# Optimization experiments

Hardware: AMD Instinct MI355X
Metric: run time of the kernel (lower is better)

The kernel has to match this reference:

```python
import jax, jax.numpy as jnp
import numpy as np

D_MODEL = 2048
NUM_HEADS = 16
NUM_KV_HEADS = 4
D_HEAD = D_MODEL // NUM_HEADS  # 128
GROUPS = NUM_HEADS // NUM_KV_HEADS  # 4
ROPE_THETA = 10000.0
EPS = 1e-6


def setup_inputs() -> dict:
    key = jax.random.key(0)
    ks = jax.random.split(key, 7)
    B, S = 2, 2048
    s = 1.0 / np.sqrt(D_MODEL)
    return {
        "qkv": jax.random.normal(ks[0], (B, S, D_MODEL), dtype=jnp.float32),
        "Wq": jax.random.normal(ks[1], (D_MODEL, D_MODEL), dtype=jnp.float32) * s,
        "Wk": jax.random.normal(ks[2], (NUM_KV_HEADS * D_HEAD, D_MODEL), dtype=jnp.float32) * s,
        "Wv": jax.random.normal(ks[3], (NUM_KV_HEADS * D_HEAD, D_MODEL), dtype=jnp.float32) * s,
        "Wo": jax.random.normal(ks[4], (D_MODEL, D_MODEL), dtype=jnp.float32) * s,
        "q_gamma": jnp.ones((D_HEAD,), dtype=jnp.float32),
        "k_gamma": jnp.ones((D_HEAD,), dtype=jnp.float32),
    }


def _rmsnorm(x, gamma):
    # per-head RMSNorm over last dim (d_head)
    var = jnp.mean(jnp.square(x), axis=-1, keepdims=True)
    return x * jax.lax.rsqrt(var + EPS) * gamma


def _rope(x, cos, sin):
    # x: [B, S, H, Dh]; cos/sin: [S, Dh]
    half = x.shape[-1] // 2
    x1, x2 = x[..., :half], x[..., half:]
    rot = jnp.concatenate([-x2, x1], axis=-1)
    return x * cos[None, :, None, :] + rot * sin[None, :, None, :]


def reference(qkv, Wq, Wk, Wv, Wo, q_gamma, k_gamma):
    B, S, D = qkv.shape
    q = jnp.einsum("bsd,ed->bse", qkv, Wq).reshape(B, S, NUM_HEADS, D_HEAD)
    k = jnp.einsum("bsd,ed->bse", qkv, Wk).reshape(B, S, NUM_KV_HEADS, D_HEAD)
    v = jnp.einsum("bsd,ed->bse", qkv, Wv).reshape(B, S, NUM_KV_HEADS, D_HEAD)

    q = _rmsnorm(q, q_gamma)
    k = _rmsnorm(k, k_gamma)

    # RoPE, position_ids = arange(S)
    pos = jnp.arange(S, dtype=jnp.float32)
    inv_freq = 1.0 / (ROPE_THETA ** (jnp.arange(0, D_HEAD, 2, dtype=jnp.float32) / D_HEAD))
    ang = pos[:, None] * inv_freq[None, :]                 # [S, Dh/2]
    cos = jnp.concatenate([jnp.cos(ang), jnp.cos(ang)], axis=-1)  # [S, Dh]
    sin = jnp.concatenate([jnp.sin(ang), jnp.sin(ang)], axis=-1)
    q = _rope(q, cos, sin)
    k = _rope(k, cos, sin)

    # [B, H, S, Dh]
    q = q.transpose(0, 2, 1, 3)
    k = k.transpose(0, 2, 1, 3)
    v = v.transpose(0, 2, 1, 3)
    # GQA: repeat kv heads
    k = jnp.repeat(k, GROUPS, axis=1)
    v = jnp.repeat(v, GROUPS, axis=1)

    scale = 1.0 / np.sqrt(D_HEAD)
    scores = jnp.einsum("bhqd,bhkd->bhqk", q, k) * scale
    causal = jnp.tril(jnp.ones((S, S), dtype=bool))
    scores = jnp.where(causal[None, None], scores, jnp.finfo(scores.dtype).min)
    probs = jax.nn.softmax(scores, axis=-1)
    attended = jnp.einsum("bhqk,bhkd->bhqd", probs, v)     # [B, H, S, Dh]
    attended = attended.transpose(0, 2, 1, 3).reshape(B, S, D)
    return jnp.einsum("bsd,ed->bse", attended, Wo)
```

## Files before the change

kernel.cpp:

```cpp
#include <hip/hip_runtime.h>

#define S_LEN 2048
#define B_SZ 2
#define DMODEL 2048
#define NHEADS 16
#define NKV 4
#define DHEAD 128
#define SCALE 0.08838834764831845f
#define KVB 32

typedef __bf16 bf16x8 __attribute__((ext_vector_type(8)));
typedef __bf16 bf16x4 __attribute__((ext_vector_type(4)));
typedef float f32x4 __attribute__((ext_vector_type(4)));

#define MFMA(a, b, c) __builtin_amdgcn_mfma_f32_16x16x32_bf16(a, b, c, 0, 0, 0)

__device__ __forceinline__ void gload_lds16(const __bf16* g, __bf16* l) {
    __builtin_amdgcn_global_load_lds(
        (const __attribute__((address_space(1))) unsigned int*)g,
        (__attribute__((address_space(3))) unsigned int*)l, 16, 0, 0);
}

__global__ void rope_tables_kernel(float* __restrict__ cosT, float* __restrict__ sinT) {
    int i = blockIdx.x * 256 + threadIdx.x;
    int s = i >> 6, d = i & 63;
    float freq = powf(10000.0f, -(2.0f * (float)d) / 128.0f);
    float ang = (float)s * freq;
    cosT[i] = cosf(ang);
    sinT[i] = sinf(ang);
}

__global__ __launch_bounds__(256) void convert_kernel(
    const float* __restrict__ s0, const float* __restrict__ s1,
    const float* __restrict__ s2, const float* __restrict__ s3,
    const float* __restrict__ s4,
    __bf16* __restrict__ d0, __bf16* __restrict__ d1, __bf16* __restrict__ d2,
    __bf16* __restrict__ d3, __bf16* __restrict__ d4) {
    const float* s;
    __bf16* d;
    int n8;
    switch (blockIdx.y) {
        case 0: s = s0; d = d0; n8 = (B_SZ * S_LEN * DMODEL) / 8; break;
        case 1: s = s1; d = d1; n8 = (DMODEL * DMODEL) / 8; break;
        case 2: s = s2; d = d2; n8 = (NKV * DHEAD * DMODEL) / 8; break;
        case 3: s = s3; d = d3; n8 = (NKV * DHEAD * DMODEL) / 8; break;
        default: s = s4; d = d4; n8 = (DMODEL * DMODEL) / 8; break;
    }
    for (int i = blockIdx.x * 256 + threadIdx.x; i < n8; i += 512 * 256) {
        float4 a = ((const float4*)s)[2 * i];
        float4 b = ((const float4*)s)[2 * i + 1];
        bf16x8 o = {(__bf16)a.x, (__bf16)a.y, (__bf16)a.z, (__bf16)a.w,
                    (__bf16)b.x, (__bf16)b.y, (__bf16)b.z, (__bf16)b.w};
        *(bf16x8*)&d[i * 8] = o;
    }
}

__device__ __forceinline__ void gemm_bt_bf16(const __bf16* __restrict__ A,
                                             const __bf16* __restrict__ W,
                                             float* __restrict__ C, int ldc,
                                             int bm, int bn, int K) {
    __shared__ alignas(16) __bf16 As[2][128][32];
    __shared__ alignas(16) __bf16 Bs[2][128][32];
    const int tid = threadIdx.x;
    const int lane = tid & 63;
    const int wave = tid >> 6;
    const int lr = lane & 15;
    const int lk = lane >> 4;
    const int wm = (wave >> 1) * 64;
    const int wn = (wave & 1) * 64;
    const int srow = lane >> 2;
    const int sc8 = (lane & 3) * 8;

    auto stage = [&](int bi, int k0) {
#pragma unroll
        for (int i = 0; i < 2; ++i) {
            const int row = i * 64 + wave * 16 + srow;
            gload_lds16(A + (size_t)(bm + row) * K + k0 + sc8,
                        &As[bi][0][0] + i * 2048 + wave * 512);
            gload_lds16(W + (size_t)(bn + row) * K + k0 + sc8,
                        &Bs[bi][0][0] + i * 2048 + wave * 512);
        }
    };

    f32x4 acc[4][4] = {};
    const int NT = K >> 5;

    stage(0, 0);
    __syncthreads();
    for (int t = 0; t < NT; ++t) {
        if (t + 1 < NT) stage((t + 1) & 1, (t + 1) * 32);
        const int bi = t & 1;
        bf16x8 af[4], bfr[4];
#pragma unroll
        for (int i = 0; i < 4; ++i) {
            af[i]  = *(const bf16x8*)&As[bi][wm + i * 16 + lr][lk * 8];
            bfr[i] = *(const bf16x8*)&Bs[bi][wn + i * 16 + lr][lk * 8];
        }
#pragma unroll
        for (int mi = 0; mi < 4; ++mi)
#pragma unroll
            for (int ni = 0; ni < 4; ++ni)
                acc[mi][ni] = MFMA(af[mi], bfr[ni], acc[mi][ni]);
        __syncthreads();
    }

#pragma unroll
    for (int mi = 0; mi < 4; ++mi)
#pragma unroll
        for (int ni = 0; ni < 4; ++ni)
#pragma unroll
            for (int r = 0; r < 4; ++r) {
                int row = bm + wm + mi * 16 + lk * 4 + r;
                int col = bn + wn + ni * 16 + lr;
                C[(size_t)row * ldc + col] = acc[mi][ni][r];
            }
}

__global__ __launch_bounds__(256) void qkv_proj_kernel(
    const __bf16* __restrict__ qkvb, const __bf16* __restrict__ Wq,
    const __bf16* __restrict__ Wk, const __bf16* __restrict__ Wv,
    float* __restrict__ q_tmp, float* __restrict__ k_tmp, float* __restrict__ v_tmp) {
    int bm = blockIdx.x * 128;
    int ny = blockIdx.y;
    const __bf16* W;
    float* C;
    int ldc, bn;
    if (ny < 16)      { W = Wq; C = q_tmp; ldc = 2048; bn = ny * 128; }
    else if (ny < 20) { W = Wk; C = k_tmp; ldc = 512;  bn = (ny - 16) * 128; }
    else              { W = Wv; C = v_tmp; ldc = 512;  bn = (ny - 20) * 128; }
    gemm_bt_bf16(qkvb, W, C, ldc, bm, bn, 2048);
}

__global__ __launch_bounds__(256) void out_proj_kernel(
    const __bf16* __restrict__ att, const __bf16* __restrict__ Wo,
    float* __restrict__ out) {
    gemm_bt_bf16(att, Wo, out, 2048, blockIdx.x * 128, blockIdx.y * 128, 2048);
}

__global__ __launch_bounds__(256) void postproc_kernel(
    const float* __restrict__ q_tmp, const float* __restrict__ k_tmp,
    const float* __restrict__ qg, const float* __restrict__ kg,
    const float* __restrict__ cosT, const float* __restrict__ sinT,
    __bf16* __restrict__ qb, __bf16* __restrict__ kb) {
    int bs = blockIdx.x;
    int b = bs >> 11, s = bs & 2047;
    int wave = threadIdx.x >> 6, lane = threadIdx.x & 63;
    float c  = cosT[s * 64 + lane];
    float sn = sinT[s * 64 + lane];
    float g1q = qg[lane], g2q = qg[lane + 64];
    float g1k = kg[lane], g2k = kg[lane + 64];

    for (int h = wave; h < NHEADS; h += 4) {
        const float* row = q_tmp + (size_t)bs * 2048 + h * 128;
        float x1 = row[lane], x2 = row[lane + 64];
        float ss = x1 * x1 + x2 * x2;
#pragma unroll
        for (int m = 1; m < 64; m <<= 1) ss += __shfl_xor(ss, m);
        float rs = rsqrtf(ss * (1.0f / 128.0f) + 1e-6f);
        float n1 = x1 * rs * g1q, n2 = x2 * rs * g2q;
        float y1 = (n1 * c - n2 * sn) * SCALE;
        float y2 = (n2 * c + n1 * sn) * SCALE;
        __bf16* orow = qb + (((size_t)(b * NHEADS + h)) * S_LEN + s) * DHEAD;
        orow[lane] = (__bf16)y1;
        orow[lane + 64] = (__bf16)y2;
    }
    int h = wave;
    if (h < NKV) {
        const float* row = k_tmp + (size_t)bs * 512 + h * 128;
        float x1 = row[lane], x2 = row[lane + 64];
        float ss = x1 * x1 + x2 * x2;
#pragma unroll
        for (int m = 1; m < 64; m <<= 1) ss += __shfl_xor(ss, m);
        float rs = rsqrtf(ss * (1.0f / 128.0f) + 1e-6f);
        float n1 = x1 * rs * g1k, n2 = x2 * rs * g2k;
        float y1 = n1 * c - n2 * sn;
        float y2 = n2 * c + n1 * sn;
        __bf16* orow = kb + (((size_t)(b * NKV + h)) * S_LEN + s) * DHEAD;
        orow[lane] = (__bf16)y1;
        orow[lane + 64] = (__bf16)y2;
    }
}

__global__ __launch_bounds__(256) void v_transpose_kernel(
    const float* __restrict__ v_tmp, __bf16* __restrict__ vt) {
    int bkv = blockIdx.x;
    int b = bkv >> 2, kvh = bkv & 3;
    int s0 = blockIdx.y * 64, d0 = blockIdx.z * 64;
    __shared__ float tile[64][65];
#pragma unroll
    for (int i = 0; i < 16; ++i) {
        int idx = threadIdx.x + i * 256;
        int r = idx >> 6, cc = idx & 63;
        tile[r][cc] = v_tmp[((size_t)(b * S_LEN) + s0 + r) * 512 + kvh * 128 + d0 + cc];
    }
    __syncthreads();
#pragma unroll
    for (int i = 0; i < 16; ++i) {
        int idx = threadIdx.x + i * 256;
        int r = idx >> 6, cc = idx & 63;
        vt[((size_t)bkv * DHEAD + d0 + r) * S_LEN + s0 + cc] = (__bf16)tile[cc][r];
    }
}

__global__ __launch_bounds__(256, 2) void flash_kernel(
    const __bf16* __restrict__ qb, const __bf16* __restrict__ kb,
    const __bf16* __restrict__ vt, __bf16* __restrict__ att) {
    __shared__ alignas(16) __bf16 K_lds[2][32 * 128];
    __shared__ alignas(16) __bf16 V_lds[2][128 * 32];
    __shared__ alignas(16) __bf16 p_lds[4][16][40];

    const int bh = blockIdx.x;
    const int b = bh >> 4, h = bh & 15, kv = h >> 2;
    const int j = blockIdx.y;
    const int lane = threadIdx.x & 63, wave = threadIdx.x >> 6;
    const int lr = lane & 15, lk = lane >> 4;

    const int qloB = j * 64 + wave * 16;
    const int qhiB = (31 - j) * 64 + wave * 16;
    const int ntL  = ((qloB + 15) >> 5) + 1;
    const int ntHw = ((qhiB + 15) >> 5) + 1;
    const int ntH  = 64 - 2 * j;

    const __bf16* Qp = qb + ((size_t)(b * NHEADS + h)) * S_LEN * DHEAD;
    const __bf16* Kp = kb + ((size_t)(b * NKV + kv)) * S_LEN * DHEAD;
    const __bf16* Vt = vt + ((size_t)(b * NKV + kv)) * DHEAD * S_LEN;

    bf16x8 qlo[4], qhi[4];
#pragma unroll
    for (int f = 0; f < 4; ++f) {
        qlo[f] = *(const bf16x8*)&Qp[(size_t)(qloB + lr) * DHEAD + f * 32 + lk * 8];
        qhi[f] = *(const bf16x8*)&Qp[(size_t)(qhiB + lr) * DHEAD + f * 32 + lk * 8];
    }

    const int c0 = 2 * wave;
    const int l4 = lane >> 4, l15 = lane & 15;
    const int l2 = lane >> 2, l3 = lane & 3;
    const int vcol = ((l3 ^ (l2 & 3)) << 3);

    auto stage = [&](int bufi, int t) {
        const int k0s = t * KVB;
#pragma unroll
        for (int i = 0; i < 2; ++i) {
            const int c = c0 + i;
            const int rK = c * 4 + l4;
            const int kcol = ((l15 ^ (rK & 7)) << 3);
            gload_lds16(Kp + (size_t)(k0s + rK) * DHEAD + kcol, &K_lds[bufi][c * 512]);
            const int rV = c * 16 + l2;
            gload_lds16(Vt + (size_t)rV * S_LEN + k0s + vcol, &V_lds[bufi][c * 512]);
        }
    };

    f32x4 accL[8] = {}, accH[8] = {};
    float lsumL[4] = {0.f, 0.f, 0.f, 0.f}, lsumH[4] = {0.f, 0.f, 0.f, 0.f};
    const int swzK = (lr & 7) << 4;
    const int swzV = (lr & 3) << 4;

    auto frag_step = [&](const bf16x8 (&qf)[4], int qbase, f32x4 (&acc)[8],
                         float (&lsum)[4], const bf16x8 (&kf)[8],
                         const bf16x8 (&vf)[8], int k0) {
        f32x4 sc[2] = {};
#pragma unroll
        for (int kk = 0; kk < 2; ++kk)
#pragma unroll
            for (int f = 0; f < 4; ++f)
                sc[kk] = MFMA(qf[f], kf[kk * 4 + f], sc[kk]);
        asm volatile("s_waitcnt lgkmcnt(0)" ::: "memory");
#pragma unroll
        for (int r = 0; r < 4; ++r) {
            const int qr = qbase + lk * 4 + r;
            float s0 = sc[0][r], s1 = sc[1][r];
            if (k0 + lr > qr) s0 = -1e30f;
            if (k0 + 16 + lr > qr) s1 = -1e30f;
            float p0 = __expf(s0), p1 = __expf(s1);
            lsum[r] += p0 + p1;
            p_lds[wave][lk * 4 + r][lr] = (__bf16)p0;
            p_lds[wave][lk * 4 + r][lr + 16] = (__bf16)p1;
        }
        asm volatile("s_waitcnt lgkmcnt(0)" ::: "memory");
        bf16x8 pf = *(const bf16x8*)&p_lds[wave][lr][lk * 8];
#pragma unroll
        for (int nf = 0; nf < 8; ++nf)
            acc[nf] = MFMA(pf, vf[nf], acc[nf]);
    };

    int cur = 0;
    stage(0, 0);
    __syncthreads();
    for (int t = 0; t < ntH; ++t) {
        if (t + 1 < ntH) stage(cur ^ 1, t + 1);
        const int k0 = t * KVB;
        bf16x8 kf[8], vf[8];
#pragma unroll
        for (int kk = 0; kk < 2; ++kk)
#pragma unroll
            for (int f = 0; f < 4; ++f) {
                const int cb = (f * 64 + lk * 16) ^ swzK;
                kf[kk * 4 + f] =
                    *(const bf16x8*)((const char*)&K_lds[cur][(kk * 16 + lr) * 128] + cb);
            }
#pragma unroll
        for (int nf = 0; nf < 8; ++nf) {
            const int cb = (lk * 16) ^ swzV;
            vf[nf] = *(const bf16x8*)((const char*)&V_lds[cur][(nf * 16 + lr) * 32] + cb);
        }
        if (t < ntHw) frag_step(qhi, qhiB, accH, lsumH, kf, vf, k0);
        if (t < ntL)  frag_step(qlo, qloB, accL, lsumL, kf, vf, k0);
        __syncthreads();
        cur ^= 1;
    }

#pragma unroll
    for (int r = 0; r < 4; ++r) {
#pragma unroll
        for (int m = 1; m < 16; m <<= 1) {
            lsumL[r] += __shfl_xor(lsumL[r], m);
            lsumH[r] += __shfl_xor(lsumH[r], m);
        }
    }
#pragma unroll
    for (int nf = 0; nf < 8; ++nf)
#pragma unroll
        for (int r = 0; r < 4; ++r) {
            int qrL = qloB + lk * 4 + r;
            int qrH = qhiB + lk * 4 + r;
            att[((size_t)(b * S_LEN) + qrL) * DMODEL + h * DHEAD + nf * 16 + lr] =
                (__bf16)(accL[nf][r] / lsumL[r]);
            att[((size_t)(b * S_LEN) + qrH) * DMODEL + h * DHEAD + nf * 16 + lr] =
                (__bf16)(accH[nf][r] / lsumH[r]);
        }
}

extern "C" void kernel_launch(void* const* d_in, const int* in_sizes, int n_in,
                              void* d_out, int out_size, void* d_ws, size_t ws_size,
                              hipStream_t stream) {
    const float* qkv = (const float*)d_in[0];
    const float* Wq  = (const float*)d_in[1];
    const float* Wk  = (const float*)d_in[2];
    const float* Wv  = (const float*)d_in[3];
    const float* Wo  = (const float*)d_in[4];
    const float* qg  = (const float*)d_in[5];
    const float* kg  = (const float*)d_in[6];
    float* out = (float*)d_out;

    size_t off = 0;
    char* wsb = (char*)d_ws;
    auto alloc = [&](size_t n) {
        char* p = wsb + off;
        off += (n + 255) & ~(size_t)255;
        return (void*)p;
    };
    const size_t M = (size_t)B_SZ * S_LEN;
    float* cosT  = (float*)alloc((size_t)S_LEN * 64 * 4);
    float* sinT  = (float*)alloc((size_t)S_LEN * 64 * 4);
    float* q_tmp = (float*)alloc(M * 2048 * 4);
    float* k_tmp = (float*)alloc(M * 512 * 4);
    float* v_tmp = (float*)alloc(M * 512 * 4);
    __bf16* qb   = (__bf16*)alloc((size_t)B_SZ * NHEADS * S_LEN * DHEAD * 2);
    __bf16* kb   = (__bf16*)alloc((size_t)B_SZ * NKV * S_LEN * DHEAD * 2);
    __bf16* vt   = (__bf16*)alloc((size_t)B_SZ * NKV * DHEAD * S_LEN * 2);
    __bf16* att  = (__bf16*)alloc(M * DMODEL * 2);
    __bf16* wo_b = (__bf16*)alloc((size_t)DMODEL * DMODEL * 2);
    __bf16* qkv_b = att;
    __bf16* wq_b  = qb;
    __bf16* wk_b  = vt;
    __bf16* wv_b  = wk_b + (size_t)NKV * DHEAD * DMODEL;

    rope_tables_kernel<<<(S_LEN * 64) / 256, 256, 0, stream>>>(cosT, sinT);
    convert_kernel<<<dim3(512, 5), 256, 0, stream>>>(qkv, Wq, Wk, Wv, Wo,
                                                     qkv_b, wq_b, wk_b, wv_b, wo_b);
    qkv_proj_kernel<<<dim3(M / 128, 24), 256, 0, stream>>>(qkv_b, wq_b, wk_b, wv_b,
                                                           q_tmp, k_tmp, v_tmp);
    postproc_kernel<<<dim3(M), 256, 0, stream>>>(q_tmp, k_tmp, qg, kg, cosT, sinT, qb, kb);
    v_transpose_kernel<<<dim3(B_SZ * NKV, S_LEN / 64, DHEAD / 64), 256, 0, stream>>>(v_tmp, vt);
    flash_kernel<<<dim3(B_SZ * NHEADS, 16), 256, 0, stream>>>(qb, kb, vt, att);
    out_proj_kernel<<<dim3(M / 128, DMODEL / 128), 256, 0, stream>>>(att, wo_b, out);
}
```

Before: 230.9 us.

## Fuse RMSNorm, RoPE and V transpose into QKV projection epilogue

Changes the GEMM wave tiling from 2x2 (64x64 per wave) to 4x1, so each wave owns 32 full rows across all 128 columns, one complete head. That lets the QKV projection epilogue compute per-head RMSNorm and RoPE in registers and write bf16 Q/K, and write V directly transposed. This drops the fp32 q/k/v scratch round trip and the separate postproc and transpose kernels. Costs: each wave now loads all 8 B fragments per k-step (more LDS reads), the epilogue stores are scattered 2-byte writes, and workspace buffers are no longer aliased.

```diff
diff --git a/kernel.cpp b/kernel.cpp
--- a/kernel.cpp
+++ b/kernel.cpp
@@ -55,10 +55,10 @@
     }
 }
 
-__device__ __forceinline__ void gemm_bt_bf16(const __bf16* __restrict__ A,
-                                             const __bf16* __restrict__ W,
-                                             float* __restrict__ C, int ldc,
-                                             int bm, int bn, int K) {
+__device__ __forceinline__ void gemm_main(const __bf16* __restrict__ A,
+                                          const __bf16* __restrict__ W,
+                                          int bm, int bn, int K,
+                                          f32x4 (&acc)[2][8]) {
     __shared__ alignas(16) __bf16 As[2][128][32];
     __shared__ alignas(16) __bf16 Bs[2][128][32];
     const int tid = threadIdx.x;
@@ -66,8 +66,6 @@
     const int wave = tid >> 6;
     const int lr = lane & 15;
     const int lk = lane >> 4;
-    const int wm = (wave >> 1) * 64;
-    const int wn = (wave & 1) * 64;
     const int srow = lane >> 2;
     const int sc8 = (lane & 3) * 8;
 
@@ -82,124 +80,127 @@
         }
     };
 
-    f32x4 acc[4][4] = {};
+#pragma unroll
+    for (int mi = 0; mi < 2; ++mi)
+#pragma unroll
+        for (int ni = 0; ni < 8; ++ni) acc[mi][ni] = (f32x4){0.f, 0.f, 0.f, 0.f};
+
     const int NT = K >> 5;
-
     stage(0, 0);
     __syncthreads();
     for (int t = 0; t < NT; ++t) {
         if (t + 1 < NT) stage((t + 1) & 1, (t + 1) * 32);
         const int bi = t & 1;
-        bf16x8 af[4], bfr[4];
-#pragma unroll
-        for (int i = 0; i < 4; ++i) {
-            af[i]  = *(const bf16x8*)&As[bi][wm + i * 16 + lr][lk * 8];
-            bfr[i] = *(const bf16x8*)&Bs[bi][wn + i * 16 + lr][lk * 8];
-        }
-#pragma unroll
-        for (int mi = 0; mi < 4; ++mi)
-#pragma unroll
-            for (int ni = 0; ni < 4; ++ni)
+        bf16x8 af[2], bfr[8];
+#pragma unroll
+        for (int i = 0; i < 2; ++i)
+            af[i] = *(const bf16x8*)&As[bi][wave * 32 + i * 16 + lr][lk * 8];
+#pragma unroll
+        for (int i = 0; i < 8; ++i)
+            bfr[i] = *(const bf16x8*)&Bs[bi][i * 16 + lr][lk * 8];
+#pragma unroll
+        for (int mi = 0; mi < 2; ++mi)
+#pragma unroll
+            for (int ni = 0; ni < 8; ++ni)
                 acc[mi][ni] = MFMA(af[mi], bfr[ni], acc[mi][ni]);
         __syncthreads();
     }
-
-#pragma unroll
-    for (int mi = 0; mi < 4; ++mi)
-#pragma unroll
-        for (int ni = 0; ni < 4; ++ni)
-#pragma unroll
-            for (int r = 0; r < 4; ++r) {
-                int row = bm + wm + mi * 16 + lk * 4 + r;
-                int col = bn + wn + ni * 16 + lr;
-                C[(size_t)row * ldc + col] = acc[mi][ni][r];
-            }
 }
 
 __global__ __launch_bounds__(256) void qkv_proj_kernel(
     const __bf16* __restrict__ qkvb, const __bf16* __restrict__ Wq,
     const __bf16* __restrict__ Wk, const __bf16* __restrict__ Wv,
-    float* __restrict__ q_tmp, float* __restrict__ k_tmp, float* __restrict__ v_tmp) {
-    int bm = blockIdx.x * 128;
-    int ny = blockIdx.y;
+    const float* __restrict__ qg, const float* __restrict__ kg,
+    const float* __restrict__ cosT, const float* __restrict__ sinT,
+    __bf16* __restrict__ qb, __bf16* __restrict__ kb, __bf16* __restrict__ vt) {
+    const int bm = blockIdx.x * 128;
+    const int ny = blockIdx.y;
     const __bf16* W;
-    float* C;
-    int ldc, bn;
-    if (ny < 16)      { W = Wq; C = q_tmp; ldc = 2048; bn = ny * 128; }
-    else if (ny < 20) { W = Wk; C = k_tmp; ldc = 512;  bn = (ny - 16) * 128; }
-    else              { W = Wv; C = v_tmp; ldc = 512;  bn = (ny - 20) * 128; }
-    gemm_bt_bf16(qkvb, W, C, ldc, bm, bn, 2048);
+    int bn;
+    if (ny < 16)      { W = Wq; bn = ny * 128; }
+    else if (ny < 20) { W = Wk; bn = (ny - 16) * 128; }
+    else              { W = Wv; bn = (ny - 20) * 128; }
+
+    f32x4 acc[2][8];
+    gemm_main(qkvb, W, bm, bn, 2048, acc);
+
+    const int lane = threadIdx.x & 63, wave = threadIdx.x >> 6;
+    const int lr = lane & 15, lk = lane >> 4;
+
+    if (ny < 20) {
+        const bool isQ = (ny < 16);
+        const float* gamma = isQ ? qg : kg;
+        const float scl = isQ ? SCALE : 1.0f;
+        __bf16* outb;
+        if (isQ) outb = qb;
+        else     outb = kb;
+        const int hh = isQ ? ny : (ny - 16);
+        const int nh = isQ ? NHEADS : NKV;
+        float g[8];
+#pragma unroll
+        for (int ni = 0; ni < 8; ++ni) g[ni] = gamma[ni * 16 + lr];
+#pragma unroll
+        for (int mi = 0; mi < 2; ++mi)
+#pragma unroll
+            for (int r = 0; r < 4; ++r) {
+                const int row = wave * 32 + mi * 16 + lk * 4 + r;
+                float ss = 0.f;
+#pragma unroll
+                for (int ni = 0; ni < 8; ++ni) ss += acc[mi][ni][r] * acc[mi][ni][r];
+                ss += __shfl_xor(ss, 1);
+                ss += __shfl_xor(ss, 2);
+                ss += __shfl_xor(ss, 4);
+                ss += __shfl_xor(ss, 8);
+                const float rs = rsqrtf(ss * (1.0f / 128.0f) + 1e-6f) * scl;
+                const int gm = bm + row, b = gm >> 11, s = gm & 2047;
+                const float* ct = cosT + s * 64;
+                const float* st = sinT + s * 64;
+                __bf16* orow = outb + (((size_t)(b * nh + hh)) * S_LEN + s) * DHEAD;
+#pragma unroll
+                for (int ni = 0; ni < 4; ++ni) {
+                    const int dm = ni * 16 + lr;
+                    const float c = ct[dm], sn = st[dm];
+                    const float n1 = acc[mi][ni][r] * rs * g[ni];
+                    const float n2 = acc[mi][ni + 4][r] * rs * g[ni + 4];
+                    orow[dm]      = (__bf16)(n1 * c - n2 * sn);
+                    orow[dm + 64] = (__bf16)(n2 * c + n1 * sn);
+                }
+            }
+    } else {
+        const int kvh = ny - 20;
+#pragma unroll
+        for (int mi = 0; mi < 2; ++mi) {
+            const int row0 = wave * 32 + mi * 16 + lk * 4;
+            const int gm = bm + row0, b = gm >> 11, s0 = gm & 2047;
+            __bf16* vbase = vt + ((size_t)(b * NKV + kvh)) * DHEAD * S_LEN;
+#pragma unroll
+            for (int ni = 0; ni < 8; ++ni) {
+                const int d = ni * 16 + lr;
+                bf16x4 pk = {(__bf16)acc[mi][ni][0], (__bf16)acc[mi][ni][1],
+                             (__bf16)acc[mi][ni][2], (__bf16)acc[mi][ni][3]};
+                *(bf16x4*)&vbase[(size_t)d * S_LEN + s0] = pk;
+            }
+        }
+    }
 }
 
 __global__ __launch_bounds__(256) void out_proj_kernel(
     const __bf16* __restrict__ att, const __bf16* __restrict__ Wo,
     float* __restrict__ out) {
-    gemm_bt_bf16(att, Wo, out, 2048, blockIdx.x * 128, blockIdx.y * 128, 2048);
-}
-
-__global__ __launch_bounds__(256) void postproc_kernel(
-    const float* __restrict__ q_tmp, const float* __restrict__ k_tmp,
-    const float* __restrict__ qg, const float* __restrict__ kg,
-    const float* __restrict__ cosT, const float* __restrict__ sinT,
-    __bf16* __restrict__ qb, __bf16* __restrict__ kb) {
-    int bs = blockIdx.x;
-    int b = bs >> 11, s = bs & 2047;
-    int wave = threadIdx.x >> 6, lane = threadIdx.x & 63;
-    float c  = cosT[s * 64 + lane];
-    float sn = sinT[s * 64 + lane];
-    float g1q = qg[lane], g2q = qg[lane + 64];
-    float g1k = kg[lane], g2k = kg[lane + 64];
-
-    for (int h = wave; h < NHEADS; h += 4) {
-        const float* row = q_tmp + (size_t)bs * 2048 + h * 128;
-        float x1 = row[lane], x2 = row[lane + 64];
-        float ss = x1 * x1 + x2 * x2;
-#pragma unroll
-        for (int m = 1; m < 64; m <<= 1) ss += __shfl_xor(ss, m);
-        float rs = rsqrtf(ss * (1.0f / 128.0f) + 1e-6f);
-        float n1 = x1 * rs * g1q, n2 = x2 * rs * g2q;
-        float y1 = (n1 * c - n2 * sn) * SCALE;
-        float y2 = (n2 * c + n1 * sn) * SCALE;
-        __bf16* orow = qb + (((size_t)(b * NHEADS + h)) * S_LEN + s) * DHEAD;
-        orow[lane] = (__bf16)y1;
-        orow[lane + 64] = (__bf16)y2;
-    }
-    int h = wave;
-    if (h < NKV) {
-        const float* row = k_tmp + (size_t)bs * 512 + h * 128;
-        float x1 = row[lane], x2 = row[lane + 64];
-        float ss = x1 * x1 + x2 * x2;
-#pragma unroll
-        for (int m = 1; m < 64; m <<= 1) ss += __shfl_xor(ss, m);
-        float rs = rsqrtf(ss * (1.0f / 128.0f) + 1e-6f);
-        float n1 = x1 * rs * g1k, n2 = x2 * rs * g2k;
-        float y1 = n1 * c - n2 * sn;
-        float y2 = n2 * c + n1 * sn;
-        __bf16* orow = kb + (((size_t)(b * NKV + h)) * S_LEN + s) * DHEAD;
-        orow[lane] = (__bf16)y1;
-        orow[lane + 64] = (__bf16)y2;
-    }
-}
-
-__global__ __launch_bounds__(256) void v_transpose_kernel(
-    const float* __restrict__ v_tmp, __bf16* __restrict__ vt) {
-    int bkv = blockIdx.x;
-    int b = bkv >> 2, kvh = bkv & 3;
-    int s0 = blockIdx.y * 64, d0 = blockIdx.z * 64;
-    __shared__ float tile[64][65];
-#pragma unroll
-    for (int i = 0; i < 16; ++i) {
-        int idx = threadIdx.x + i * 256;
-        int r = idx >> 6, cc = idx & 63;
-        tile[r][cc] = v_tmp[((size_t)(b * S_LEN) + s0 + r) * 512 + kvh * 128 + d0 + cc];
-    }
-    __syncthreads();
-#pragma unroll
-    for (int i = 0; i < 16; ++i) {
-        int idx = threadIdx.x + i * 256;
-        int r = idx >> 6, cc = idx & 63;
-        vt[((size_t)bkv * DHEAD + d0 + r) * S_LEN + s0 + cc] = (__bf16)tile[cc][r];
-    }
+    const int bm = blockIdx.x * 128, bn = blockIdx.y * 128;
+    f32x4 acc[2][8];
+    gemm_main(att, Wo, bm, bn, 2048, acc);
+    const int lane = threadIdx.x & 63, wave = threadIdx.x >> 6;
+    const int lr = lane & 15, lk = lane >> 4;
+#pragma unroll
+    for (int mi = 0; mi < 2; ++mi)
+#pragma unroll
+        for (int ni = 0; ni < 8; ++ni)
+#pragma unroll
+            for (int r = 0; r < 4; ++r) {
+                const int row = wave * 32 + mi * 16 + lk * 4 + r;
+                out[(size_t)(bm + row) * DMODEL + bn + ni * 16 + lr] = acc[mi][ni][r];
+            }
 }
 
 __global__ __launch_bounds__(256, 2) void flash_kernel(
@@ -350,28 +351,23 @@
         return (void*)p;
     };
     const size_t M = (size_t)B_SZ * S_LEN;
-    float* cosT  = (float*)alloc((size_t)S_LEN * 64 * 4);
-    float* sinT  = (float*)alloc((size_t)S_LEN * 64 * 4);
-    float* q_tmp = (float*)alloc(M * 2048 * 4);
-    float* k_tmp = (float*)alloc(M * 512 * 4);
-    float* v_tmp = (float*)alloc(M * 512 * 4);
-    __bf16* qb   = (__bf16*)alloc((size_t)B_SZ * NHEADS * S_LEN * DHEAD * 2);
-    __bf16* kb   = (__bf16*)alloc((size_t)B_SZ * NKV * S_LEN * DHEAD * 2);
-    __bf16* vt   = (__bf16*)alloc((size_t)B_SZ * NKV * DHEAD * S_LEN * 2);
-    __bf16* att  = (__bf16*)alloc(M * DMODEL * 2);
-    __bf16* wo_b = (__bf16*)alloc((size_t)DMODEL * DMODEL * 2);
-    __bf16* qkv_b = att;
-    __bf16* wq_b  = qb;
-    __bf16* wk_b  = vt;
-    __bf16* wv_b  = wk_b + (size_t)NKV * DHEAD * DMODEL;
+    float* cosT   = (float*)alloc((size_t)S_LEN * 64 * 4);
+    float* sinT   = (float*)alloc((size_t)S_LEN * 64 * 4);
+    __bf16* qb    = (__bf16*)alloc((size_t)B_SZ * NHEADS * S_LEN * DHEAD * 2);
+    __bf16* kb    = (__bf16*)alloc((size_t)B_SZ * NKV * S_LEN * DHEAD * 2);
+    __bf16* vt    = (__bf16*)alloc((size_t)B_SZ * NKV * DHEAD * S_LEN * 2);
+    __bf16* att   = (__bf16*)alloc(M * DMODEL * 2);
+    __bf16* qkv_b = (__bf16*)alloc(M * DMODEL * 2);
+    __bf16* wq_b  = (__bf16*)alloc((size_t)DMODEL * DMODEL * 2);
+    __bf16* wk_b  = (__bf16*)alloc((size_t)NKV * DHEAD * DMODEL * 2);
+    __bf16* wv_b  = (__bf16*)alloc((size_t)NKV * DHEAD * DMODEL * 2);
+    __bf16* wo_b  = (__bf16*)alloc((size_t)DMODEL * DMODEL * 2);
 
     rope_tables_kernel<<<(S_LEN * 64) / 256, 256, 0, stream>>>(cosT, sinT);
     convert_kernel<<<dim3(512, 5), 256, 0, stream>>>(qkv, Wq, Wk, Wv, Wo,
                                                      qkv_b, wq_b, wk_b, wv_b, wo_b);
-    qkv_proj_kernel<<<dim3(M / 128, 24), 256, 0, stream>>>(qkv_b, wq_b, wk_b, wv_b,
-                                                           q_tmp, k_tmp, v_tmp);
-    postproc_kernel<<<dim3(M), 256, 0, stream>>>(q_tmp, k_tmp, qg, kg, cosT, sinT, qb, kb);
-    v_transpose_kernel<<<dim3(B_SZ * NKV, S_LEN / 64, DHEAD / 64), 256, 0, stream>>>(v_tmp, vt);
+    qkv_proj_kernel<<<dim3(M / 128, 24), 256, 0, stream>>>(
+        qkv_b, wq_b, wk_b, wv_b, qg, kg, cosT, sinT, qb, kb, vt);
     flash_kernel<<<dim3(B_SZ * NHEADS, 16), 256, 0, stream>>>(qb, kb, vt, att);
-    out_proj_kernel<<<dim3(M / 128, DMODEL / 128), 256, 0, stream>>>(att, wo_b, out);
-}
+    out_proj_kernel<<<dim3(M / 128, 16), 256, 0, stream>>>(att, wo_b, out);
+}
```

Result: slower. 260.4 us (+12.8%).

## Rewrite projection GEMMs with 256-wide tiles, swizzled LDS, and deeper prefetch

Applied to the files above, without the earlier changes.

Replaces the 128x128 BF16 GEMM core used by the QKV and output projections with a templated 256-column tile kernel. It uses 512 threads, a K-step of 64, an XOR-swizzled LDS layout against bank conflicts, and two-stage prefetch with explicit vmcnt waits and raw barriers. Block IDs are remapped so tiles are spread across XCDs. The aim is more data reuse per tile and less load latency exposed. In exchange it uses more LDS and registers, and the QKV grid shrinks to 192 blocks, which may underfill the 256 CUs.

```diff
diff --git a/kernel.cpp b/kernel.cpp
--- a/kernel.cpp
+++ b/kernel.cpp
@@ -55,86 +55,151 @@
     }
 }
 
-__device__ __forceinline__ void gemm_bt_bf16(const __bf16* __restrict__ A,
-                                             const __bf16* __restrict__ W,
-                                             float* __restrict__ C, int ldc,
-                                             int bm, int bn, int K) {
-    __shared__ alignas(16) __bf16 As[2][128][32];
-    __shared__ alignas(16) __bf16 Bs[2][128][32];
+template <int BM>
+__device__ __forceinline__ void gemm256(const __bf16* __restrict__ A,
+                                        const __bf16* __restrict__ W,
+                                        int bm, int bn, int K,
+                                        f32x4 (&acc)[BM / 32][4]) {
+    constexpr int MI = BM / 32;
+    constexpr int ALT = BM / 64;
+    __shared__ alignas(16) __bf16 As[2][BM * 64];
+    __shared__ alignas(16) __bf16 Bs[2][256 * 64];
     const int tid = threadIdx.x;
     const int lane = tid & 63;
     const int wave = tid >> 6;
-    const int lr = lane & 15;
-    const int lk = lane >> 4;
-    const int wm = (wave >> 1) * 64;
-    const int wn = (wave & 1) * 64;
-    const int srow = lane >> 2;
-    const int sc8 = (lane & 3) * 8;
-
-    auto stage = [&](int bi, int k0) {
-#pragma unroll
-        for (int i = 0; i < 2; ++i) {
-            const int row = i * 64 + wave * 16 + srow;
-            gload_lds16(A + (size_t)(bm + row) * K + k0 + sc8,
-                        &As[bi][0][0] + i * 2048 + wave * 512);
-            gload_lds16(W + (size_t)(bn + row) * K + k0 + sc8,
-                        &Bs[bi][0][0] + i * 2048 + wave * 512);
+    const int lr = lane & 15, lk = lane >> 4;
+    const int wr = wave >> 2;
+    const int wc = wave & 3;
+    const int sRow = lane >> 3;
+    const int sCol = 8 * ((lane & 7) ^ sRow);
+
+    auto stageA = [&](int bi, int k0) {
+#pragma unroll
+        for (int it = 0; it < ALT; ++it) {
+            const int row = it * 64 + wave * 8 + sRow;
+            gload_lds16(A + (size_t)(bm + row) * K + k0 + sCol,
+                        &As[bi][it * 4096 + wave * 512]);
         }
     };
-
-    f32x4 acc[4][4] = {};
-    const int NT = K >> 5;
-
-    stage(0, 0);
-    __syncthreads();
+    auto stageB = [&](int bi, int k0) {
+#pragma unroll
+        for (int it = 0; it < 4; ++it) {
+            const int row = it * 64 + wave * 8 + sRow;
+            gload_lds16(W + (size_t)(bn + row) * K + k0 + sCol,
+                        &Bs[bi][it * 4096 + wave * 512]);
+        }
+    };
+
+#pragma unroll
+    for (int mi = 0; mi < MI; ++mi)
+#pragma unroll
+        for (int ni = 0; ni < 4; ++ni) acc[mi][ni] = (f32x4){0.f, 0.f, 0.f, 0.f};
+
+    const int NT = K >> 6;
+    stageA(0, 0);
+    stageB(0, 0);
+    stageA(1, 64);
+    stageB(1, 64);
+    if constexpr (BM == 256) asm volatile("s_waitcnt vmcnt(8)" ::: "memory");
+    else                     asm volatile("s_waitcnt vmcnt(6)" ::: "memory");
+    __builtin_amdgcn_s_barrier();
+
     for (int t = 0; t < NT; ++t) {
-        if (t + 1 < NT) stage((t + 1) & 1, (t + 1) * 32);
         const int bi = t & 1;
-        bf16x8 af[4], bfr[4];
-#pragma unroll
-        for (int i = 0; i < 4; ++i) {
-            af[i]  = *(const bf16x8*)&As[bi][wm + i * 16 + lr][lk * 8];
-            bfr[i] = *(const bf16x8*)&Bs[bi][wn + i * 16 + lr][lk * 8];
-        }
-#pragma unroll
-        for (int mi = 0; mi < 4; ++mi)
-#pragma unroll
-            for (int ni = 0; ni < 4; ++ni)
-                acc[mi][ni] = MFMA(af[mi], bfr[ni], acc[mi][ni]);
-        __syncthreads();
-    }
-
-#pragma unroll
-    for (int mi = 0; mi < 4; ++mi)
-#pragma unroll
-        for (int ni = 0; ni < 4; ++ni)
-#pragma unroll
-            for (int r = 0; r < 4; ++r) {
-                int row = bm + wm + mi * 16 + lk * 4 + r;
-                int col = bn + wn + ni * 16 + lr;
-                C[(size_t)row * ldc + col] = acc[mi][ni][r];
-            }
-}
-
-__global__ __launch_bounds__(256) void qkv_proj_kernel(
+#pragma unroll
+        for (int kk = 0; kk < 2; ++kk) {
+            bf16x8 af[MI], bfr[4];
+#pragma unroll
+            for (int i = 0; i < MI; ++i) {
+                const int r = wr * (BM / 2) + i * 16 + lr;
+                const int slot = (kk * 4 + lk) ^ (r & 7);
+                af[i] = *(const bf16x8*)&As[bi][r * 64 + slot * 8];
+            }
+#pragma unroll
+            for (int i = 0; i < 4; ++i) {
+                const int r = wc * 64 + i * 16 + lr;
+                const int slot = (kk * 4 + lk) ^ (r & 7);
+                bfr[i] = *(const bf16x8*)&Bs[bi][r * 64 + slot * 8];
+            }
+#pragma unroll
+            for (int mi = 0; mi < MI; ++mi)
+#pragma unroll
+                for (int ni = 0; ni < 4; ++ni)
+                    acc[mi][ni] = MFMA(af[mi], bfr[ni], acc[mi][ni]);
+        }
+        asm volatile("s_waitcnt lgkmcnt(0)" ::: "memory");
+        __builtin_amdgcn_sched_barrier(0);
+        __builtin_amdgcn_s_barrier();
+        if (t + 2 < NT) {
+            stageA(bi, (t + 2) * 64);
+            stageB(bi, (t + 2) * 64);
+        }
+        if (t + 1 < NT) {
+            if (t + 2 < NT) {
+                if constexpr (BM == 256) asm volatile("s_waitcnt vmcnt(8)" ::: "memory");
+                else                     asm volatile("s_waitcnt vmcnt(6)" ::: "memory");
+            } else {
+                asm volatile("s_waitcnt vmcnt(0)" ::: "memory");
+            }
+            __builtin_amdgcn_s_barrier();
+        }
+    }
+}
+
+__global__ __launch_bounds__(512, 2) void qkv_proj_kernel(
     const __bf16* __restrict__ qkvb, const __bf16* __restrict__ Wq,
     const __bf16* __restrict__ Wk, const __bf16* __restrict__ Wv,
     float* __restrict__ q_tmp, float* __restrict__ k_tmp, float* __restrict__ v_tmp) {
-    int bm = blockIdx.x * 128;
-    int ny = blockIdx.y;
+    const int id = (blockIdx.x & 7) * 24 + (blockIdx.x >> 3);
+    const int bmi = id / 12, bni = id % 12;
+    const int bm = bmi * 256;
     const __bf16* W;
     float* C;
     int ldc, bn;
-    if (ny < 16)      { W = Wq; C = q_tmp; ldc = 2048; bn = ny * 128; }
-    else if (ny < 20) { W = Wk; C = k_tmp; ldc = 512;  bn = (ny - 16) * 128; }
-    else              { W = Wv; C = v_tmp; ldc = 512;  bn = (ny - 20) * 128; }
-    gemm_bt_bf16(qkvb, W, C, ldc, bm, bn, 2048);
-}
-
-__global__ __launch_bounds__(256) void out_proj_kernel(
+    if (bni < 8)       { W = Wq; C = q_tmp; ldc = 2048; bn = bni * 256; }
+    else if (bni < 10) { W = Wk; C = k_tmp; ldc = 512;  bn = (bni - 8) * 256; }
+    else               { W = Wv; C = v_tmp; ldc = 512;  bn = (bni - 10) * 256; }
+
+    f32x4 acc[8][4];
+    gemm256<256>(qkvb, W, bm, bn, 2048, acc);
+
+    const int lane = threadIdx.x & 63, wave = threadIdx.x >> 6;
+    const int lr = lane & 15, lk = lane >> 4;
+    const int wr = wave >> 2, wc = wave & 3;
+#pragma unroll
+    for (int mi = 0; mi < 8; ++mi)
+#pragma unroll
+        for (int ni = 0; ni < 4; ++ni)
+#pragma unroll
+            for (int r = 0; r < 4; ++r) {
+                const int row = bm + wr * 128 + mi * 16 + lk * 4 + r;
+                const int col = bn + wc * 64 + ni * 16 + lr;
+                C[(size_t)row * ldc + col] = acc[mi][ni][r];
+            }
+}
+
+__global__ __launch_bounds__(512, 2) void out_proj_kernel(
     const __bf16* __restrict__ att, const __bf16* __restrict__ Wo,
     float* __restrict__ out) {
-    gemm_bt_bf16(att, Wo, out, 2048, blockIdx.x * 128, blockIdx.y * 128, 2048);
+    const int id = (blockIdx.x & 7) * 32 + (blockIdx.x >> 3);
+    const int bm = (id >> 3) * 128, bn = (id & 7) * 256;
+
+    f32x4 acc[4][4];
+    gemm256<128>(att, Wo, bm, bn, 2048, acc);
+
+    const int lane = threadIdx.x & 63, wave = threadIdx.x >> 6;
+    const int lr = lane & 15, lk = lane >> 4;
+    const int wr = wave >> 2, wc = wave & 3;
+#pragma unroll
+    for (int mi = 0; mi < 4; ++mi)
+#pragma unroll
+        for (int ni = 0; ni < 4; ++ni)
+#pragma unroll
+            for (int r = 0; r < 4; ++r) {
+                const int row = bm + wr * 64 + mi * 16 + lk * 4 + r;
+                const int col = bn + wc * 64 + ni * 16 + lr;
+                out[(size_t)row * DMODEL + col] = acc[mi][ni][r];
+            }
 }
 
 __global__ __launch_bounds__(256) void postproc_kernel(
@@ -368,10 +433,10 @@
     rope_tables_kernel<<<(S_LEN * 64) / 256, 256, 0, stream>>>(cosT, sinT);
     convert_kernel<<<dim3(512, 5), 256, 0, stream>>>(qkv, Wq, Wk, Wv, Wo,
                                                      qkv_b, wq_b, wk_b, wv_b, wo_b);
-    qkv_proj_kernel<<<dim3(M / 128, 24), 256, 0, stream>>>(qkv_b, wq_b, wk_b, wv_b,
-                                                           q_tmp, k_tmp, v_tmp);
+    qkv_proj_kernel<<<192, 512, 0, stream>>>(qkv_b, wq_b, wk_b, wv_b,
+                                             q_tmp, k_tmp, v_tmp);
     postproc_kernel<<<dim3(M), 256, 0, stream>>>(q_tmp, k_tmp, qg, kg, cosT, sinT, qb, kb);
     v_transpose_kernel<<<dim3(B_SZ * NKV, S_LEN / 64, DHEAD / 64), 256, 0, stream>>>(v_tmp, vt);
     flash_kernel<<<dim3(B_SZ * NHEADS, 16), 256, 0, stream>>>(qb, kb, vt, att);
-    out_proj_kernel<<<dim3(M / 128, DMODEL / 128), 256, 0, stream>>>(att, wo_b, out);
-}
+    out_proj_kernel<<<256, 512, 0, stream>>>(att, wo_b, out);
+}
```

New measurement: 211.5 us. -8.4%, faster.
